# Optimization experiments

Measured on AMD Instinct MI355X. Metric: run time of the kernel, lower is better.

## Reference

```python
import jax, jax.numpy as jnp
import numpy as np

N, IN, H, OUT, C = 1024, 64, 64, 64, 32
EPS = 1e-5   # SAKELayer.epsilon
INF = 1e5    # SAKELayer.inf


def _w(key, i, o, scale=1.0):
    return jax.random.normal(key, (i, o), jnp.float32) * (scale / np.sqrt(i))


def setup_inputs() -> dict:
    key = jax.random.key(0)
    ks = jax.random.split(key, 16)
    return dict(
        h=jax.random.normal(ks[0], (N, IN), jnp.float32),
        x=jax.random.normal(ks[1], (N, 3), jnp.float32),
        # edge model (ConcatenationFilter): Linear(2*IN+1,H), SiLU, Linear(H,H)
        ew1=_w(ks[2], 2 * IN + 1, H), eb1=jnp.zeros((H,), jnp.float32),
        ew2=_w(ks[3], H, H), eb2=jnp.zeros((H,), jnp.float32),
        # node_mlp: Linear(2H+IN,H), SiLU, Linear(H,OUT)
        nw1=_w(ks[4], 2 * H + IN, H), nb1=jnp.zeros((H,), jnp.float32),
        nw2=_w(ks[5], H, OUT), nb2=jnp.zeros((OUT,), jnp.float32),
        # coordinate_mlp: Linear(H,H), SiLU, Linear(H,1,bias=False) xavier gain 1e-3
        cw1=_w(ks[6], H, H), cb1=jnp.zeros((H,), jnp.float32),
        cw2=_w(ks[7], H, 1, scale=1e-3),
        # semantic_attention_mlp: Linear(H,1), LeakyReLU
        aw=_w(ks[8], H, 1), ab=jnp.zeros((1,), jnp.float32),
        # coefficients_mlp: Linear(H,H), SiLU, Linear(H,C)
        fw1=_w(ks[9], H, H), fb1=jnp.zeros((H,), jnp.float32),
        fw2=_w(ks[10], H, C), fb2=jnp.zeros((C,), jnp.float32),
        # post_norm_mlp: Linear(C,H), SiLU, Linear(H,H)
        pw1=_w(ks[11], C, H), pb1=jnp.zeros((H,), jnp.float32),
        pw2=_w(ks[12], H, H), pb2=jnp.zeros((H,), jnp.float32),
        log_gamma=jnp.array(0.0, jnp.float32),
    )


def reference(h, x, ew1, eb1, ew2, eb2, nw1, nb1, nw2, nb2, cw1, cb1, cw2,
              aw, ab, fw1, fb1, fw2, fb2, pw1, pb1, pw2, pb2, log_gamma):
    n, d_in = h.shape
    silu = jax.nn.silu
    eye = jnp.eye(n, dtype=h.dtype)[:, :, None]                    # [n,n,1]

    x_minus_xt = x[:, None, :] - x[None, :, :]                     # [n,n,3]
    norm = jnp.sqrt(jnp.sum(x_minus_xt ** 2, -1, keepdims=True) + EPS)  # [n,n,1]

    h_cat_ht = jnp.concatenate(
        [jnp.broadcast_to(h[:, None, :], (n, n, d_in)),
         jnp.broadcast_to(h[None, :, :], (n, n, d_in))], -1)       # [n,n,2*IN]

    # edge model: MLP over concat(features, distance)
    e_in = jnp.concatenate([h_cat_ht, norm], -1)                   # [n,n,2*IN+1]
    h_e = silu(e_in @ ew1 + eb1) @ ew2 + eb2                       # [n,n,H]

    # euclidean attention over neighbors j (diag masked by +INF distance)
    att_e = jax.nn.softmax(-(norm + INF * eye) * jnp.exp(log_gamma), axis=1)
    # semantic attention
    att_s = jax.nn.softmax(jax.nn.leaky_relu(h_e @ aw + ab) - INF * eye, axis=1)
    comb = att_e * att_s
    comb = comb / (jnp.sum(comb, axis=1, keepdims=True) + EPS)     # [n,n,1]
    h_e_att = h_e * comb                                           # [n,n,H]

    # spatial attention: equivariant coefficient combinations
    coeff = silu(h_e_att @ fw1 + fb1) @ fw2 + fb2                  # [n,n,C]
    dirs = x_minus_xt / (norm + 1.0)                               # [n,n,3]
    combos = jnp.einsum('ijc,ijd->icd', coeff, dirs) / n           # mean over j -> [n,C,3]
    h_comb = silu(jnp.sum(combos ** 2, -1) @ pw1 + pb1) @ pw2 + pb2  # [n,H]

    # node update
    h_agg = jnp.sum(h_e_att, axis=1)                               # [n,H]
    node_in = jnp.concatenate([h, h_agg, h_comb], -1)              # [n,2H+IN]
    h_out = h + (silu(node_in @ nw1 + nb1) @ nw2 + nb2)            # residual

    # equivariant coordinate update
    phi = silu(h_e @ cw1 + cb1) @ cw2                              # [n,n,1]
    x_out = x + jnp.mean(x_minus_xt * phi, axis=1)                 # [n,3]
    return h_out, x_out
```

## Files before the change

### kernel.cpp

```cpp
#include <hip/hip_runtime.h>
#include <hip/hip_bf16.h>

#define NN 1024
#define JT 128
#define LSTR 72
#define EPSV 1e-5f
#define BIGINF 1e5f

typedef __attribute__((ext_vector_type(8))) short short8;
typedef __attribute__((ext_vector_type(4))) short short4v;
typedef __attribute__((ext_vector_type(4))) float f32x4;

__device__ __forceinline__ float siluf(float v) {
    return v * __builtin_amdgcn_rcpf(1.0f + __expf(-v));
}
__device__ __forceinline__ float pnorm(float dx, float dy, float dz) {
    return sqrtf(dx * dx + dy * dy + dz * dz + EPSV);
}
__device__ __forceinline__ float wsum(float v) {
#pragma unroll
    for (int off = 32; off > 0; off >>= 1) v += __shfl_xor(v, off, 64);
    return v;
}
__device__ __forceinline__ float red16(float v) {
    v += __shfl_xor(v, 1, 64); v += __shfl_xor(v, 2, 64);
    v += __shfl_xor(v, 4, 64); v += __shfl_xor(v, 8, 64);
    return v;
}
__device__ __forceinline__ float redquad(float v) {
    v += __shfl_xor(v, 16, 64); v += __shfl_xor(v, 32, 64);
    return v;
}
__device__ __forceinline__ short f2bs(float v) {
    __hip_bfloat16 b = __float2bfloat16(v);
    return *reinterpret_cast<short*>(&b);
}
__device__ __forceinline__ short f2bt(float v) {
    return (short)(__float_as_uint(v) >> 16);
}

__global__ void kA(const float* __restrict__ h, const float* __restrict__ ew1,
                   const float* __restrict__ eb1, const float* __restrict__ ew2,
                   const float* __restrict__ cw1, const float* __restrict__ fw1,
                   const float* __restrict__ fw2, const float* __restrict__ aw,
                   const float* __restrict__ ab, const float* __restrict__ eb2,
                   float* __restrict__ HA, float* __restrict__ HB,
                   float* __restrict__ HBT, short* __restrict__ ew2T,
                   short* __restrict__ cw1T, short* __restrict__ fw1T,
                   short* __restrict__ fw2T, float* __restrict__ wsv,
                   float* __restrict__ svb) {
    const int b = blockIdx.x;
    const int o = threadIdx.x;
    if (b < NN) {
        const int i = b;
        float hv = h[i * 64 + o];
        float a = 0.f, bb = eb1[o];
#pragma unroll
        for (int k = 0; k < 64; k++) {
            float hk = __shfl(hv, k, 64);
            a += hk * ew1[k * 64 + o];
            bb += hk * ew1[(64 + k) * 64 + o];
        }
        HA[i * 64 + o] = a;
        HB[i * 64 + o] = bb;
        HBT[o * NN + i] = bb;
    } else if (b < NN + 64) {
        const int r = b - NN;
        ew2T[r * 64 + o] = f2bs(ew2[o * 64 + r]);
        cw1T[r * 64 + o] = f2bs(cw1[o * 64 + r]);
        fw1T[r * 64 + o] = f2bs(fw1[o * 64 + r]);
        if (r < 32) fw2T[r * 64 + o] = f2bs(fw2[o * 32 + r]);
    } else {
        float s = 0.f;
#pragma unroll
        for (int q = 0; q < 64; q++) s += ew2[o * 64 + q] * aw[q];
        wsv[o] = s;
        float e = wsum(eb2[o] * aw[o]);
        if (o == 0) svb[0] = e + ab[0];
    }
}

__global__ __launch_bounds__(256) void kBn(
    const float* __restrict__ x, const float* __restrict__ ew1,
    const float* __restrict__ HA, const float* __restrict__ HBT,
    const float* __restrict__ wsv, const float* __restrict__ svb,
    const float* __restrict__ lg, float* __restrict__ ls,
    float* __restrict__ rowm, float* __restrict__ rowd) {
    const int i = blockIdx.x;
    const int t = threadIdx.x;
    const float* HAi = HA + i * 64;
    const float* w1 = ew1 + 128 * 64;
    const float gamma = __expf(lg[0]);
    const float svb0 = svb[0];
    const float xi0 = x[i * 3 + 0], xi1 = x[i * 3 + 1], xi2 = x[i * 3 + 2];

    float4 xa = ((const float4*)x)[3 * t + 0];
    float4 xb = ((const float4*)x)[3 * t + 1];
    float4 xc = ((const float4*)x)[3 * t + 2];
    float nrm[4], le[4], lv[4];
    {
        float dx0 = xi0 - xa.x, dy0 = xi1 - xa.y, dz0 = xi2 - xa.z;
        float dx1 = xi0 - xa.w, dy1 = xi1 - xb.x, dz1 = xi2 - xb.y;
        float dx2 = xi0 - xb.z, dy2 = xi1 - xb.w, dz2 = xi2 - xc.x;
        float dx3 = xi0 - xc.y, dy3 = xi1 - xc.z, dz3 = xi2 - xc.w;
        nrm[0] = pnorm(dx0, dy0, dz0);
        nrm[1] = pnorm(dx1, dy1, dz1);
        nrm[2] = pnorm(dx2, dy2, dz2);
        nrm[3] = pnorm(dx3, dy3, dz3);
    }
    float d0 = 0.f, d1 = 0.f, d2 = 0.f, d3 = 0.f;
#pragma unroll 8
    for (int k = 0; k < 64; k++) {
        float4 hb = *(const float4*)&HBT[k * NN + 4 * t];
        float hk = HAi[k], w1k = w1[k], wv = wsv[k];
        d0 += siluf(hk + hb.x + nrm[0] * w1k) * wv;
        d1 += siluf(hk + hb.y + nrm[1] * w1k) * wv;
        d2 += siluf(hk + hb.z + nrm[2] * w1k) * wv;
        d3 += siluf(hk + hb.w + nrm[3] * w1k) * wv;
    }
    float me = -3.0e38f, ms = -3.0e38f;
    float4 svo;
    {
        float dd[4] = {d0, d1, d2, d3};
#pragma unroll
        for (int m = 0; m < 4; m++) {
            int j = 4 * t + m;
            float sv = dd[m] + svb0;
            sv = sv >= 0.f ? sv : 0.01f * sv;
            if (j == i) sv -= BIGINF;
            lv[m] = sv;
            le[m] = -(nrm[m] + (j == i ? BIGINF : 0.f)) * gamma;
            me = fmaxf(me, le[m]);
            ms = fmaxf(ms, lv[m]);
        }
        svo.x = lv[0]; svo.y = lv[1]; svo.z = lv[2]; svo.w = lv[3];
    }
    *(float4*)&ls[(size_t)i * NN + 4 * t] = svo;

    __shared__ float sm[4], ss[4], s1[4], s2[4], s3[4];
#pragma unroll
    for (int off = 32; off > 0; off >>= 1) {
        me = fmaxf(me, __shfl_xor(me, off, 64));
        ms = fmaxf(ms, __shfl_xor(ms, off, 64));
    }
    const int w = t >> 6;
    if ((t & 63) == 0) { sm[w] = me; ss[w] = ms; }
    __syncthreads();
    me = fmaxf(fmaxf(sm[0], sm[1]), fmaxf(sm[2], sm[3]));
    ms = fmaxf(fmaxf(ss[0], ss[1]), fmaxf(ss[2], ss[3]));
    float Se = 0.f, Ss = 0.f, Sq = 0.f;
#pragma unroll
    for (int m = 0; m < 4; m++) {
        float ee = __expf(le[m] - me);
        float es = __expf(lv[m] - ms);
        Se += ee; Ss += es; Sq += ee * es;
    }
    Se = wsum(Se); Ss = wsum(Ss); Sq = wsum(Sq);
    if ((t & 63) == 0) { s1[w] = Se; s2[w] = Ss; s3[w] = Sq; }
    __syncthreads();
    if (t == 0) {
        rowm[i] = me + ms;
        rowd[i] = (s3[0] + s3[1] + s3[2] + s3[3]) +
                  EPSV * (s1[0] + s1[1] + s1[2] + s1[3]) * (s2[0] + s2[1] + s2[2] + s2[3]);
    }
}

__device__ __forceinline__ void stageW(const short* __restrict__ g, short* s,
                                       int tid, int rows) {
    for (int c = tid; c < rows * 16; c += 512) {
        int r = c >> 4, q = c & 15;
        *(short4v*)&s[r * LSTR + q * 4] = *(const short4v*)&g[r * 64 + q * 4];
    }
}

__global__ __launch_bounds__(512) void kD(
    const float* __restrict__ x, const float* __restrict__ ew1,
    const float* __restrict__ eb2, const float* __restrict__ cb1,
    const float* __restrict__ cw2, const float* __restrict__ fb1,
    const float* __restrict__ fb2, const float* __restrict__ lg,
    const float* __restrict__ HA, const float* __restrict__ HB,
    const short* __restrict__ ew2T, const short* __restrict__ cw1T,
    const short* __restrict__ fw1T, const short* __restrict__ fw2T,
    const float* __restrict__ ls, const float* __restrict__ rowm,
    const float* __restrict__ rowd, float* __restrict__ hagg,
    float* __restrict__ combos, float* __restrict__ xupd) {
    __shared__ __align__(16) short sWe[64 * LSTR];
    __shared__ __align__(16) short sWc[64 * LSTR];
    __shared__ __align__(16) short sWf[64 * LSTR];
    __shared__ __align__(16) short sW2[32 * LSTR];
    __shared__ __align__(16) short sScr[8][16 * LSTR];
    __shared__ float sHag[64], sCombos[96], sXupd[3];

    const int tid = threadIdx.x;
    const int i = blockIdx.x;
    const int jbase = blockIdx.y * JT;
    const int lane = tid & 63, w = tid >> 6;
    const int col = lane & 15, quad = lane >> 4;

    if (tid < 64) sHag[tid] = 0.f;
    else if (tid < 160) sCombos[tid - 64] = 0.f;
    else if (tid < 163) sXupd[tid - 160] = 0.f;
    stageW(ew2T, sWe, tid, 64);
    stageW(cw1T, sWc, tid, 64);
    stageW(fw1T, sWf, tid, 64);
    stageW(fw2T, sW2, tid, 32);
    __syncthreads();

    short* scr = sScr[w];
    const int jrow = jbase + w * 16 + col;
    float dxv, dyv, dzv, nrmv, combv, fxv, fyv, fzv;
    {
        dxv = x[i * 3 + 0] - x[jrow * 3 + 0];
        dyv = x[i * 3 + 1] - x[jrow * 3 + 1];
        dzv = x[i * 3 + 2] - x[jrow * 3 + 2];
        nrmv = pnorm(dxv, dyv, dzv);
        float inv1 = __builtin_amdgcn_rcpf(nrmv + 1.0f);
        fxv = dxv * inv1; fyv = dyv * inv1; fzv = dzv * inv1;
        float gamma = __expf(lg[0]);
        float le = -(nrmv + (jrow == i ? BIGINF : 0.f)) * gamma;
        combv = __expf(le + ls[(size_t)i * NN + jrow] - rowm[i]) / rowd[i];
    }

    f32x4 acc[4] = {{0.f, 0.f, 0.f, 0.f}, {0.f, 0.f, 0.f, 0.f},
                    {0.f, 0.f, 0.f, 0.f}, {0.f, 0.f, 0.f, 0.f}};
    {
        short8 afr[2];
#pragma unroll
        for (int kb = 0; kb < 2; kb++) {
            const int k0 = kb * 32 + quad * 8;
            const float* hb = &HB[jrow * 64 + k0];
            const float* ha = &HA[i * 64 + k0];
            const float* w1 = &ew1[128 * 64 + k0];
#pragma unroll
            for (int t = 0; t < 8; t++)
                afr[kb][t] = f2bt(siluf(ha[t] + hb[t] + nrmv * w1[t]));
        }
#pragma unroll
        for (int kb = 0; kb < 2; kb++) {
#pragma unroll
            for (int nb = 0; nb < 4; nb++) {
                short8 b = *(const short8*)&sWe[(nb * 16 + col) * LSTR + kb * 32 + quad * 8];
                acc[nb] = __builtin_amdgcn_mfma_f32_16x16x32_bf16(afr[kb], b, acc[nb], 0, 0, 0);
            }
        }
    }
    {
        float eb[4];
#pragma unroll
        for (int nb = 0; nb < 4; nb++) eb[nb] = eb2[nb * 16 + col];
        float hv[4][4], cmb[4];
#pragma unroll
        for (int reg = 0; reg < 4; reg++) cmb[reg] = __shfl(combv, quad * 4 + reg, 64);
#pragma unroll
        for (int reg = 0; reg < 4; reg++) {
#pragma unroll
            for (int nb = 0; nb < 4; nb++) {
                hv[nb][reg] = acc[nb][reg] + eb[nb];
                scr[(quad * 4 + reg) * LSTR + nb * 16 + col] = f2bt(hv[nb][reg]);
            }
        }
#pragma unroll
        for (int nb = 0; nb < 4; nb++) {
            float v = 0.f;
#pragma unroll
            for (int reg = 0; reg < 4; reg++) v += hv[nb][reg] * cmb[reg];
            v = redquad(v);
            if (quad == 0) atomicAdd(&sHag[nb * 16 + col], v);
        }
    }
    short8 a0 = *(const short8*)&scr[col * LSTR + quad * 8];
    short8 a1 = *(const short8*)&scr[col * LSTR + 32 + quad * 8];

    {
        f32x4 p[4] = {{0.f, 0.f, 0.f, 0.f}, {0.f, 0.f, 0.f, 0.f},
                      {0.f, 0.f, 0.f, 0.f}, {0.f, 0.f, 0.f, 0.f}};
#pragma unroll
        for (int nb = 0; nb < 4; nb++) {
            short8 b0 = *(const short8*)&sWc[(nb * 16 + col) * LSTR + quad * 8];
            short8 b1 = *(const short8*)&sWc[(nb * 16 + col) * LSTR + 32 + quad * 8];
            p[nb] = __builtin_amdgcn_mfma_f32_16x16x32_bf16(a0, b0, p[nb], 0, 0, 0);
            p[nb] = __builtin_amdgcn_mfma_f32_16x16x32_bf16(a1, b1, p[nb], 0, 0, 0);
        }
        float cbv[4], cwv[4];
#pragma unroll
        for (int nb = 0; nb < 4; nb++) { cbv[nb] = cb1[nb * 16 + col]; cwv[nb] = cw2[nb * 16 + col]; }
        float xa0 = 0.f, xa1 = 0.f, xa2 = 0.f;
#pragma unroll
        for (int reg = 0; reg < 4; reg++) {
            float ph = 0.f;
#pragma unroll
            for (int nb = 0; nb < 4; nb++) ph += siluf(p[nb][reg] + cbv[nb]) * cwv[nb];
            ph = red16(ph);
            float tdx = __shfl(dxv, quad * 4 + reg, 64);
            float tdy = __shfl(dyv, quad * 4 + reg, 64);
            float tdz = __shfl(dzv, quad * 4 + reg, 64);
            if (col == 0) { xa0 += ph * tdx; xa1 += ph * tdy; xa2 += ph * tdz; }
        }
        xa0 = wsum(xa0); xa1 = wsum(xa1); xa2 = wsum(xa2);
        if (lane == 0) {
            atomicAdd(&sXupd[0], xa0);
            atomicAdd(&sXupd[1], xa1);
            atomicAdd(&sXupd[2], xa2);
        }
    }

    {
        f32x4 vacc[4] = {{0.f, 0.f, 0.f, 0.f}, {0.f, 0.f, 0.f, 0.f},
                         {0.f, 0.f, 0.f, 0.f}, {0.f, 0.f, 0.f, 0.f}};
#pragma unroll
        for (int nb = 0; nb < 4; nb++) {
            short8 b0 = *(const short8*)&sWf[(nb * 16 + col) * LSTR + quad * 8];
            short8 b1 = *(const short8*)&sWf[(nb * 16 + col) * LSTR + 32 + quad * 8];
            vacc[nb] = __builtin_amdgcn_mfma_f32_16x16x32_bf16(a0, b0, vacc[nb], 0, 0, 0);
            vacc[nb] = __builtin_amdgcn_mfma_f32_16x16x32_bf16(a1, b1, vacc[nb], 0, 0, 0);
        }
        float fbv[4], cmb[4];
#pragma unroll
        for (int nb = 0; nb < 4; nb++) fbv[nb] = fb1[nb * 16 + col];
#pragma unroll
        for (int reg = 0; reg < 4; reg++) cmb[reg] = __shfl(combv, quad * 4 + reg, 64);
#pragma unroll
        for (int reg = 0; reg < 4; reg++) {
#pragma unroll
            for (int nb = 0; nb < 4; nb++)
                scr[(quad * 4 + reg) * LSTR + nb * 16 + col] =
                    f2bt(siluf(cmb[reg] * vacc[nb][reg] + fbv[nb]));
        }
    }
    short8 wa0 = *(const short8*)&scr[col * LSTR + quad * 8];
    short8 wa1 = *(const short8*)&scr[col * LSTR + 32 + quad * 8];

    {
        f32x4 cacc[2] = {{0.f, 0.f, 0.f, 0.f}, {0.f, 0.f, 0.f, 0.f}};
#pragma unroll
        for (int nb = 0; nb < 2; nb++) {
            short8 b0 = *(const short8*)&sW2[(nb * 16 + col) * LSTR + quad * 8];
            short8 b1 = *(const short8*)&sW2[(nb * 16 + col) * LSTR + 32 + quad * 8];
            cacc[nb] = __builtin_amdgcn_mfma_f32_16x16x32_bf16(wa0, b0, cacc[nb], 0, 0, 0);
            cacc[nb] = __builtin_amdgcn_mfma_f32_16x16x32_bf16(wa1, b1, cacc[nb], 0, 0, 0);
        }
#pragma unroll
        for (int nb = 0; nb < 2; nb++) {
            float fb2v = fb2[nb * 16 + col];
            float px = 0.f, py = 0.f, pz = 0.f;
#pragma unroll
            for (int reg = 0; reg < 4; reg++) {
                float cf = cacc[nb][reg] + fb2v;
                float tfx = __shfl(fxv, quad * 4 + reg, 64);
                float tfy = __shfl(fyv, quad * 4 + reg, 64);
                float tfz = __shfl(fzv, quad * 4 + reg, 64);
                px += cf * tfx; py += cf * tfy; pz += cf * tfz;
            }
            px = redquad(px); py = redquad(py); pz = redquad(pz);
            if (quad == 0) {
                int c = nb * 16 + col;
                atomicAdd(&sCombos[c * 3 + 0], px);
                atomicAdd(&sCombos[c * 3 + 1], py);
                atomicAdd(&sCombos[c * 3 + 2], pz);
            }
        }
    }
    __syncthreads();
    if (tid < 64) atomicAdd(&hagg[i * 64 + tid], sHag[tid]);
    else if (tid >= 64 && tid < 160) atomicAdd(&combos[i * 96 + tid - 64], sCombos[tid - 64]);
    else if (tid >= 160 && tid < 163) atomicAdd(&xupd[i * 3 + tid - 160], sXupd[tid - 160]);
}

__global__ void kE(const float* __restrict__ h, const float* __restrict__ x,
                   const float* __restrict__ nw1, const float* __restrict__ nb1,
                   const float* __restrict__ nw2, const float* __restrict__ nb2,
                   const float* __restrict__ pw1, const float* __restrict__ pb1,
                   const float* __restrict__ pw2, const float* __restrict__ pb2,
                   const float* __restrict__ hagg, const float* __restrict__ combos,
                   const float* __restrict__ xupd, float* __restrict__ out) {
    const int i = blockIdx.x, o = threadIdx.x;
    const float invN = 1.0f / (float)NN;
    float r = 0.f;
    if (o < 32) {
        float v0 = combos[i * 96 + o * 3 + 0] * invN;
        float v1 = combos[i * 96 + o * 3 + 1] * invN;
        float v2 = combos[i * 96 + o * 3 + 2] * invN;
        r = v0 * v0 + v1 * v1 + v2 * v2;
    }
    float t1 = pb1[o];
#pragma unroll
    for (int k = 0; k < 32; k++) t1 += __shfl(r, k, 64) * pw1[k * 64 + o];
    t1 = siluf(t1);
    float hc = pb2[o];
#pragma unroll
    for (int k = 0; k < 64; k++) hc += __shfl(t1, k, 64) * pw2[k * 64 + o];
    float hi = h[i * 64 + o];
    float ha = hagg[i * 64 + o];
    float t2 = nb1[o];
#pragma unroll
    for (int k = 0; k < 64; k++) t2 += __shfl(hi, k, 64) * nw1[k * 64 + o];
#pragma unroll
    for (int k = 0; k < 64; k++) t2 += __shfl(ha, k, 64) * nw1[(64 + k) * 64 + o];
#pragma unroll
    for (int k = 0; k < 64; k++) t2 += __shfl(hc, k, 64) * nw1[(128 + k) * 64 + o];
    t2 = siluf(t2);
    float ho = hi + nb2[o];
#pragma unroll
    for (int k = 0; k < 64; k++) ho += __shfl(t2, k, 64) * nw2[k * 64 + o];
    out[i * 64 + o] = ho;
    if (o < 3)
        out[NN * 64 + i * 3 + o] = x[i * 3 + o] + xupd[i * 3 + o] * invN;
}

extern "C" void kernel_launch(void* const* d_in, const int* in_sizes, int n_in,
                              void* d_out, int out_size, void* d_ws, size_t ws_size,
                              hipStream_t stream) {
    (void)in_sizes; (void)n_in; (void)out_size; (void)ws_size;
    const float* h   = (const float*)d_in[0];
    const float* x   = (const float*)d_in[1];
    const float* ew1 = (const float*)d_in[2];
    const float* eb1 = (const float*)d_in[3];
    const float* ew2 = (const float*)d_in[4];
    const float* eb2 = (const float*)d_in[5];
    const float* nw1 = (const float*)d_in[6];
    const float* nb1 = (const float*)d_in[7];
    const float* nw2 = (const float*)d_in[8];
    const float* nb2 = (const float*)d_in[9];
    const float* cw1 = (const float*)d_in[10];
    const float* cb1 = (const float*)d_in[11];
    const float* cw2 = (const float*)d_in[12];
    const float* aw  = (const float*)d_in[13];
    const float* ab  = (const float*)d_in[14];
    const float* fw1 = (const float*)d_in[15];
    const float* fb1 = (const float*)d_in[16];
    const float* fw2 = (const float*)d_in[17];
    const float* fb2 = (const float*)d_in[18];
    const float* pw1 = (const float*)d_in[19];
    const float* pb1 = (const float*)d_in[20];
    const float* pw2 = (const float*)d_in[21];
    const float* pb2 = (const float*)d_in[22];
    const float* lg  = (const float*)d_in[23];
    float* out = (float*)d_out;

    float* W      = (float*)d_ws;
    float* ls     = W;
    float* HA     = ls + (size_t)NN * NN;
    float* HB     = HA + NN * 64;
    float* HBT    = HB + NN * 64;
    float* rowm   = HBT + NN * 64;
    float* rowd   = rowm + NN;
    float* hagg   = rowd + NN;
    float* combos = hagg + NN * 64;
    float* xupd   = combos + NN * 96;
    float* wsv    = xupd + NN * 3;
    float* svb    = wsv + 64;
    short* ew2T   = (short*)(svb + 4);
    short* cw1T   = ew2T + 64 * 64;
    short* fw1T   = cw1T + 64 * 64;
    short* fw2T   = fw1T + 64 * 64;

    hipMemsetAsync(hagg, 0, (size_t)(NN * 64 + NN * 96 + NN * 3) * sizeof(float), stream);
    kA<<<NN + 65, 64, 0, stream>>>(h, ew1, eb1, ew2, cw1, fw1, fw2, aw, ab, eb2,
                                   HA, HB, HBT, ew2T, cw1T, fw1T, fw2T, wsv, svb);
    kBn<<<NN, 256, 0, stream>>>(x, ew1, HA, HBT, wsv, svb, lg, ls, rowm, rowd);
    dim3 g2(NN, NN / JT);
    kD<<<g2, 512, 0, stream>>>(x, ew1, eb2, cb1, cw2, fb1, fb2, lg, HA, HB,
                               ew2T, cw1T, fw1T, fw2T, ls, rowm, rowd,
                               hagg, combos, xupd);
    kE<<<NN, 64, 0, stream>>>(h, x, nw1, nb1, nw2, nb2, pw1, pb1, pw2, pb2,
                              hagg, combos, xupd, out);
}
```

Before: 310.6 us.

## Make edge kernel persistent over two rows and all j-tiles, drop global atomics

The edge kernel's grid changes from (N, N/128) blocks to N/2 blocks. Each block now loops over two i rows and all eight j tiles, so the weight staging into LDS and the per-block constants are loaded once and reused. Per-row results are written straight to global memory instead of accumulated with global atomics, which also removes the memset. The cost is far fewer blocks (512 on a large GPU) and serial j-loop latency, which may lower occupancy and latency hiding.

```diff
diff --git a/kernel.cpp b/kernel.cpp
--- a/kernel.cpp
+++ b/kernel.cpp
@@ -192,178 +192,195 @@
     __shared__ float sHag[64], sCombos[96], sXupd[3];
 
     const int tid = threadIdx.x;
-    const int i = blockIdx.x;
-    const int jbase = blockIdx.y * JT;
     const int lane = tid & 63, w = tid >> 6;
     const int col = lane & 15, quad = lane >> 4;
 
-    if (tid < 64) sHag[tid] = 0.f;
-    else if (tid < 160) sCombos[tid - 64] = 0.f;
-    else if (tid < 163) sXupd[tid - 160] = 0.f;
     stageW(ew2T, sWe, tid, 64);
     stageW(cw1T, sWc, tid, 64);
     stageW(fw1T, sWf, tid, 64);
     stageW(fw2T, sW2, tid, 32);
+
+    short* scr = sScr[w];
+    const float gamma = __expf(lg[0]);
+
+    float w1r[2][8];
+#pragma unroll
+    for (int kb = 0; kb < 2; kb++)
+#pragma unroll
+        for (int t = 0; t < 8; t++)
+            w1r[kb][t] = ew1[128 * 64 + kb * 32 + quad * 8 + t];
+    float eb[4], cbv[4], cwv[4], fbv[4];
+#pragma unroll
+    for (int nb = 0; nb < 4; nb++) {
+        eb[nb] = eb2[nb * 16 + col];
+        cbv[nb] = cb1[nb * 16 + col];
+        cwv[nb] = cw2[nb * 16 + col];
+        fbv[nb] = fb1[nb * 16 + col];
+    }
+    float fb2v[2] = {fb2[col], fb2[16 + col]};
     __syncthreads();
 
-    short* scr = sScr[w];
-    const int jrow = jbase + w * 16 + col;
-    float dxv, dyv, dzv, nrmv, combv, fxv, fyv, fzv;
-    {
-        dxv = x[i * 3 + 0] - x[jrow * 3 + 0];
-        dyv = x[i * 3 + 1] - x[jrow * 3 + 1];
-        dzv = x[i * 3 + 2] - x[jrow * 3 + 2];
-        nrmv = pnorm(dxv, dyv, dzv);
-        float inv1 = __builtin_amdgcn_rcpf(nrmv + 1.0f);
-        fxv = dxv * inv1; fyv = dyv * inv1; fzv = dzv * inv1;
-        float gamma = __expf(lg[0]);
-        float le = -(nrmv + (jrow == i ? BIGINF : 0.f)) * gamma;
-        combv = __expf(le + ls[(size_t)i * NN + jrow] - rowm[i]) / rowd[i];
-    }
-
-    f32x4 acc[4] = {{0.f, 0.f, 0.f, 0.f}, {0.f, 0.f, 0.f, 0.f},
-                    {0.f, 0.f, 0.f, 0.f}, {0.f, 0.f, 0.f, 0.f}};
-    {
-        short8 afr[2];
-#pragma unroll
-        for (int kb = 0; kb < 2; kb++) {
-            const int k0 = kb * 32 + quad * 8;
-            const float* hb = &HB[jrow * 64 + k0];
-            const float* ha = &HA[i * 64 + k0];
-            const float* w1 = &ew1[128 * 64 + k0];
+#pragma unroll 1
+    for (int ii = 0; ii < 2; ii++) {
+        const int i = blockIdx.x * 2 + ii;
+        if (tid < 64) sHag[tid] = 0.f;
+        else if (tid < 160) sCombos[tid - 64] = 0.f;
+        else if (tid < 163) sXupd[tid - 160] = 0.f;
+        float har[2][8];
+#pragma unroll
+        for (int kb = 0; kb < 2; kb++)
 #pragma unroll
             for (int t = 0; t < 8; t++)
-                afr[kb][t] = f2bt(siluf(ha[t] + hb[t] + nrmv * w1[t]));
+                har[kb][t] = HA[i * 64 + kb * 32 + quad * 8 + t];
+        const float rm = rowm[i];
+        const float invd = 1.0f / rowd[i];
+        const float xi0 = x[i * 3 + 0], xi1 = x[i * 3 + 1], xi2 = x[i * 3 + 2];
+        const float* lsi = ls + (size_t)i * NN;
+        __syncthreads();
+
+#pragma unroll 1
+        for (int jt = 0; jt < 8; jt++) {
+            const int jrow = jt * JT + w * 16 + col;
+            float dxv = xi0 - x[jrow * 3 + 0];
+            float dyv = xi1 - x[jrow * 3 + 1];
+            float dzv = xi2 - x[jrow * 3 + 2];
+            float nrmv = pnorm(dxv, dyv, dzv);
+            float inv1 = __builtin_amdgcn_rcpf(nrmv + 1.0f);
+            float fxv = dxv * inv1, fyv = dyv * inv1, fzv = dzv * inv1;
+            float le = -(nrmv + (jrow == i ? BIGINF : 0.f)) * gamma;
+            float combv = __expf(le + lsi[jrow] - rm) * invd;
+
+            short8 afr[2];
+#pragma unroll
+            for (int kb = 0; kb < 2; kb++) {
+                const float* hb = &HB[jrow * 64 + kb * 32 + quad * 8];
+#pragma unroll
+                for (int t = 0; t < 8; t++)
+                    afr[kb][t] = f2bt(siluf(har[kb][t] + hb[t] + nrmv * w1r[kb][t]));
+            }
+            f32x4 acc[4] = {{0.f, 0.f, 0.f, 0.f}, {0.f, 0.f, 0.f, 0.f},
+                            {0.f, 0.f, 0.f, 0.f}, {0.f, 0.f, 0.f, 0.f}};
+#pragma unroll
+            for (int kb = 0; kb < 2; kb++) {
+#pragma unroll
+                for (int nb = 0; nb < 4; nb++) {
+                    short8 b = *(const short8*)&sWe[(nb * 16 + col) * LSTR + kb * 32 + quad * 8];
+                    acc[nb] = __builtin_amdgcn_mfma_f32_16x16x32_bf16(afr[kb], b, acc[nb], 0, 0, 0);
+                }
+            }
+            {
+                float hv[4][4], cmb[4];
+#pragma unroll
+                for (int reg = 0; reg < 4; reg++) cmb[reg] = __shfl(combv, quad * 4 + reg, 64);
+#pragma unroll
+                for (int reg = 0; reg < 4; reg++) {
+#pragma unroll
+                    for (int nb = 0; nb < 4; nb++) {
+                        hv[nb][reg] = acc[nb][reg] + eb[nb];
+                        scr[(quad * 4 + reg) * LSTR + nb * 16 + col] = f2bt(hv[nb][reg]);
+                    }
+                }
+#pragma unroll
+                for (int nb = 0; nb < 4; nb++) {
+                    float v = 0.f;
+#pragma unroll
+                    for (int reg = 0; reg < 4; reg++) v += hv[nb][reg] * cmb[reg];
+                    v = redquad(v);
+                    if (quad == 0) atomicAdd(&sHag[nb * 16 + col], v);
+                }
+            }
+            short8 a0 = *(const short8*)&scr[col * LSTR + quad * 8];
+            short8 a1 = *(const short8*)&scr[col * LSTR + 32 + quad * 8];
+
+            {
+                f32x4 p[4] = {{0.f, 0.f, 0.f, 0.f}, {0.f, 0.f, 0.f, 0.f},
+                              {0.f, 0.f, 0.f, 0.f}, {0.f, 0.f, 0.f, 0.f}};
+#pragma unroll
+                for (int nb = 0; nb < 4; nb++) {
+                    short8 b0 = *(const short8*)&sWc[(nb * 16 + col) * LSTR + quad * 8];
+                    short8 b1 = *(const short8*)&sWc[(nb * 16 + col) * LSTR + 32 + quad * 8];
+                    p[nb] = __builtin_amdgcn_mfma_f32_16x16x32_bf16(a0, b0, p[nb], 0, 0, 0);
+                    p[nb] = __builtin_amdgcn_mfma_f32_16x16x32_bf16(a1, b1, p[nb], 0, 0, 0);
+                }
+                float xa0 = 0.f, xa1 = 0.f, xa2 = 0.f;
+#pragma unroll
+                for (int reg = 0; reg < 4; reg++) {
+                    float ph = 0.f;
+#pragma unroll
+                    for (int nb = 0; nb < 4; nb++) ph += siluf(p[nb][reg] + cbv[nb]) * cwv[nb];
+                    ph = red16(ph);
+                    float tdx = __shfl(dxv, quad * 4 + reg, 64);
+                    float tdy = __shfl(dyv, quad * 4 + reg, 64);
+                    float tdz = __shfl(dzv, quad * 4 + reg, 64);
+                    if (col == 0) { xa0 += ph * tdx; xa1 += ph * tdy; xa2 += ph * tdz; }
+                }
+                xa0 = wsum(xa0); xa1 = wsum(xa1); xa2 = wsum(xa2);
+                if (lane == 0) {
+                    atomicAdd(&sXupd[0], xa0);
+                    atomicAdd(&sXupd[1], xa1);
+                    atomicAdd(&sXupd[2], xa2);
+                }
+            }
+
+            {
+                f32x4 vacc[4] = {{0.f, 0.f, 0.f, 0.f}, {0.f, 0.f, 0.f, 0.f},
+                                 {0.f, 0.f, 0.f, 0.f}, {0.f, 0.f, 0.f, 0.f}};
+#pragma unroll
+                for (int nb = 0; nb < 4; nb++) {
+                    short8 b0 = *(const short8*)&sWf[(nb * 16 + col) * LSTR + quad * 8];
+                    short8 b1 = *(const short8*)&sWf[(nb * 16 + col) * LSTR + 32 + quad * 8];
+                    vacc[nb] = __builtin_amdgcn_mfma_f32_16x16x32_bf16(a0, b0, vacc[nb], 0, 0, 0);
+                    vacc[nb] = __builtin_amdgcn_mfma_f32_16x16x32_bf16(a1, b1, vacc[nb], 0, 0, 0);
+                }
+                float cmb[4];
+#pragma unroll
+                for (int reg = 0; reg < 4; reg++) cmb[reg] = __shfl(combv, quad * 4 + reg, 64);
+#pragma unroll
+                for (int reg = 0; reg < 4; reg++) {
+#pragma unroll
+                    for (int nb = 0; nb < 4; nb++)
+                        scr[(quad * 4 + reg) * LSTR + nb * 16 + col] =
+                            f2bt(siluf(cmb[reg] * vacc[nb][reg] + fbv[nb]));
+                }
+            }
+            short8 wa0 = *(const short8*)&scr[col * LSTR + quad * 8];
+            short8 wa1 = *(const short8*)&scr[col * LSTR + 32 + quad * 8];
+
+            {
+                f32x4 cacc[2] = {{0.f, 0.f, 0.f, 0.f}, {0.f, 0.f, 0.f, 0.f}};
+#pragma unroll
+                for (int nb = 0; nb < 2; nb++) {
+                    short8 b0 = *(const short8*)&sW2[(nb * 16 + col) * LSTR + quad * 8];
+                    short8 b1 = *(const short8*)&sW2[(nb * 16 + col) * LSTR + 32 + quad * 8];
+                    cacc[nb] = __builtin_amdgcn_mfma_f32_16x16x32_bf16(wa0, b0, cacc[nb], 0, 0, 0);
+                    cacc[nb] = __builtin_amdgcn_mfma_f32_16x16x32_bf16(wa1, b1, cacc[nb], 0, 0, 0);
+                }
+#pragma unroll
+                for (int nb = 0; nb < 2; nb++) {
+                    float px = 0.f, py = 0.f, pz = 0.f;
+#pragma unroll
+                    for (int reg = 0; reg < 4; reg++) {
+                        float cf = cacc[nb][reg] + fb2v[nb];
+                        float tfx = __shfl(fxv, quad * 4 + reg, 64);
+                        float tfy = __shfl(fyv, quad * 4 + reg, 64);
+                        float tfz = __shfl(fzv, quad * 4 + reg, 64);
+                        px += cf * tfx; py += cf * tfy; pz += cf * tfz;
+                    }
+                    px = redquad(px); py = redquad(py); pz = redquad(pz);
+                    if (quad == 0) {
+                        int c = nb * 16 + col;
+                        atomicAdd(&sCombos[c * 3 + 0], px);
+                        atomicAdd(&sCombos[c * 3 + 1], py);
+                        atomicAdd(&sCombos[c * 3 + 2], pz);
+                    }
+                }
+            }
         }
-#pragma unroll
-        for (int kb = 0; kb < 2; kb++) {
-#pragma unroll
-            for (int nb = 0; nb < 4; nb++) {
-                short8 b = *(const short8*)&sWe[(nb * 16 + col) * LSTR + kb * 32 + quad * 8];
-                acc[nb] = __builtin_amdgcn_mfma_f32_16x16x32_bf16(afr[kb], b, acc[nb], 0, 0, 0);
-            }
-        }
-    }
-    {
-        float eb[4];
-#pragma unroll
-        for (int nb = 0; nb < 4; nb++) eb[nb] = eb2[nb * 16 + col];
-        float hv[4][4], cmb[4];
-#pragma unroll
-        for (int reg = 0; reg < 4; reg++) cmb[reg] = __shfl(combv, quad * 4 + reg, 64);
-#pragma unroll
-        for (int reg = 0; reg < 4; reg++) {
-#pragma unroll
-            for (int nb = 0; nb < 4; nb++) {
-                hv[nb][reg] = acc[nb][reg] + eb[nb];
-                scr[(quad * 4 + reg) * LSTR + nb * 16 + col] = f2bt(hv[nb][reg]);
-            }
-        }
-#pragma unroll
-        for (int nb = 0; nb < 4; nb++) {
-            float v = 0.f;
-#pragma unroll
-            for (int reg = 0; reg < 4; reg++) v += hv[nb][reg] * cmb[reg];
-            v = redquad(v);
-            if (quad == 0) atomicAdd(&sHag[nb * 16 + col], v);
-        }
-    }
-    short8 a0 = *(const short8*)&scr[col * LSTR + quad * 8];
-    short8 a1 = *(const short8*)&scr[col * LSTR + 32 + quad * 8];
-
-    {
-        f32x4 p[4] = {{0.f, 0.f, 0.f, 0.f}, {0.f, 0.f, 0.f, 0.f},
-                      {0.f, 0.f, 0.f, 0.f}, {0.f, 0.f, 0.f, 0.f}};
-#pragma unroll
-        for (int nb = 0; nb < 4; nb++) {
-            short8 b0 = *(const short8*)&sWc[(nb * 16 + col) * LSTR + quad * 8];
-            short8 b1 = *(const short8*)&sWc[(nb * 16 + col) * LSTR + 32 + quad * 8];
-            p[nb] = __builtin_amdgcn_mfma_f32_16x16x32_bf16(a0, b0, p[nb], 0, 0, 0);
-            p[nb] = __builtin_amdgcn_mfma_f32_16x16x32_bf16(a1, b1, p[nb], 0, 0, 0);
-        }
-        float cbv[4], cwv[4];
-#pragma unroll
-        for (int nb = 0; nb < 4; nb++) { cbv[nb] = cb1[nb * 16 + col]; cwv[nb] = cw2[nb * 16 + col]; }
-        float xa0 = 0.f, xa1 = 0.f, xa2 = 0.f;
-#pragma unroll
-        for (int reg = 0; reg < 4; reg++) {
-            float ph = 0.f;
-#pragma unroll
-            for (int nb = 0; nb < 4; nb++) ph += siluf(p[nb][reg] + cbv[nb]) * cwv[nb];
-            ph = red16(ph);
-            float tdx = __shfl(dxv, quad * 4 + reg, 64);
-            float tdy = __shfl(dyv, quad * 4 + reg, 64);
-            float tdz = __shfl(dzv, quad * 4 + reg, 64);
-            if (col == 0) { xa0 += ph * tdx; xa1 += ph * tdy; xa2 += ph * tdz; }
-        }
-        xa0 = wsum(xa0); xa1 = wsum(xa1); xa2 = wsum(xa2);
-        if (lane == 0) {
-            atomicAdd(&sXupd[0], xa0);
-            atomicAdd(&sXupd[1], xa1);
-            atomicAdd(&sXupd[2], xa2);
-        }
-    }
-
-    {
-        f32x4 vacc[4] = {{0.f, 0.f, 0.f, 0.f}, {0.f, 0.f, 0.f, 0.f},
-                         {0.f, 0.f, 0.f, 0.f}, {0.f, 0.f, 0.f, 0.f}};
-#pragma unroll
-        for (int nb = 0; nb < 4; nb++) {
-            short8 b0 = *(const short8*)&sWf[(nb * 16 + col) * LSTR + quad * 8];
-            short8 b1 = *(const short8*)&sWf[(nb * 16 + col) * LSTR + 32 + quad * 8];
-            vacc[nb] = __builtin_amdgcn_mfma_f32_16x16x32_bf16(a0, b0, vacc[nb], 0, 0, 0);
-            vacc[nb] = __builtin_amdgcn_mfma_f32_16x16x32_bf16(a1, b1, vacc[nb], 0, 0, 0);
-        }
-        float fbv[4], cmb[4];
-#pragma unroll
-        for (int nb = 0; nb < 4; nb++) fbv[nb] = fb1[nb * 16 + col];
-#pragma unroll
-        for (int reg = 0; reg < 4; reg++) cmb[reg] = __shfl(combv, quad * 4 + reg, 64);
-#pragma unroll
-        for (int reg = 0; reg < 4; reg++) {
-#pragma unroll
-            for (int nb = 0; nb < 4; nb++)
-                scr[(quad * 4 + reg) * LSTR + nb * 16 + col] =
-                    f2bt(siluf(cmb[reg] * vacc[nb][reg] + fbv[nb]));
-        }
-    }
-    short8 wa0 = *(const short8*)&scr[col * LSTR + quad * 8];
-    short8 wa1 = *(const short8*)&scr[col * LSTR + 32 + quad * 8];
-
-    {
-        f32x4 cacc[2] = {{0.f, 0.f, 0.f, 0.f}, {0.f, 0.f, 0.f, 0.f}};
-#pragma unroll
-        for (int nb = 0; nb < 2; nb++) {
-            short8 b0 = *(const short8*)&sW2[(nb * 16 + col) * LSTR + quad * 8];
-            short8 b1 = *(const short8*)&sW2[(nb * 16 + col) * LSTR + 32 + quad * 8];
-            cacc[nb] = __builtin_amdgcn_mfma_f32_16x16x32_bf16(wa0, b0, cacc[nb], 0, 0, 0);
-            cacc[nb] = __builtin_amdgcn_mfma_f32_16x16x32_bf16(wa1, b1, cacc[nb], 0, 0, 0);
-        }
-#pragma unroll
-        for (int nb = 0; nb < 2; nb++) {
-            float fb2v = fb2[nb * 16 + col];
-            float px = 0.f, py = 0.f, pz = 0.f;
-#pragma unroll
-            for (int reg = 0; reg < 4; reg++) {
-                float cf = cacc[nb][reg] + fb2v;
-                float tfx = __shfl(fxv, quad * 4 + reg, 64);
-                float tfy = __shfl(fyv, quad * 4 + reg, 64);
-                float tfz = __shfl(fzv, quad * 4 + reg, 64);
-                px += cf * tfx; py += cf * tfy; pz += cf * tfz;
-            }
-            px = redquad(px); py = redquad(py); pz = redquad(pz);
-            if (quad == 0) {
-                int c = nb * 16 + col;
-                atomicAdd(&sCombos[c * 3 + 0], px);
-                atomicAdd(&sCombos[c * 3 + 1], py);
-                atomicAdd(&sCombos[c * 3 + 2], pz);
-            }
-        }
-    }
-    __syncthreads();
-    if (tid < 64) atomicAdd(&hagg[i * 64 + tid], sHag[tid]);
-    else if (tid >= 64 && tid < 160) atomicAdd(&combos[i * 96 + tid - 64], sCombos[tid - 64]);
-    else if (tid >= 160 && tid < 163) atomicAdd(&xupd[i * 3 + tid - 160], sXupd[tid - 160]);
+        __syncthreads();
+        if (tid < 64) hagg[i * 64 + tid] = sHag[tid];
+        else if (tid < 160) combos[i * 96 + tid - 64] = sCombos[tid - 64];
+        else if (tid < 163) xupd[i * 3 + tid - 160] = sXupd[tid - 160];
+    }
 }
 
 __global__ void kE(const float* __restrict__ h, const float* __restrict__ x,
@@ -454,14 +471,12 @@
     short* fw1T   = cw1T + 64 * 64;
     short* fw2T   = fw1T + 64 * 64;
 
-    hipMemsetAsync(hagg, 0, (size_t)(NN * 64 + NN * 96 + NN * 3) * sizeof(float), stream);
     kA<<<NN + 65, 64, 0, stream>>>(h, ew1, eb1, ew2, cw1, fw1, fw2, aw, ab, eb2,
                                    HA, HB, HBT, ew2T, cw1T, fw1T, fw2T, wsv, svb);
     kBn<<<NN, 256, 0, stream>>>(x, ew1, HA, HBT, wsv, svb, lg, ls, rowm, rowd);
-    dim3 g2(NN, NN / JT);
-    kD<<<g2, 512, 0, stream>>>(x, ew1, eb2, cb1, cw2, fb1, fb2, lg, HA, HB,
-                               ew2T, cw1T, fw1T, fw2T, ls, rowm, rowd,
-                               hagg, combos, xupd);
+    kD<<<NN / 2, 512, 0, stream>>>(x, ew1, eb2, cb1, cw2, fb1, fb2, lg, HA, HB,
+                                   ew2T, cw1T, fw1T, fw2T, ls, rowm, rowd,
+                                   hagg, combos, xupd);
     kE<<<NN, 64, 0, stream>>>(h, x, nw1, nb1, nw2, nb2, pw1, pb1, pw2, pb2,
                               hagg, combos, xupd, out);
 }
```

Result: faster. 299.8 us (-3.5%).
